# Kernel tuning notes

Hardware: AMD Instinct MI355X
Metric: run time of the kernel (lower is better)

## Reference

```python
import jax, jax.numpy as jnp
import numpy as np
from jax import lax

B, T_HIST, T_PRED = 8192, 11, 80
IN, H = 2, 64


def _glorot(key, shape, fan):
    bound = 1.0 / np.sqrt(fan)
    return jax.random.uniform(key, shape, jnp.float32, -bound, bound)


def setup_inputs() -> dict:
    key = jax.random.key(0)
    ks = jax.random.split(key, 20)
    inp = {"x": jax.random.normal(ks[0], (B, T_HIST, IN), jnp.float32)}
    # encoder / decoder: 2-layer tanh RNN, PyTorch param layout (out_features first)
    for pfx, base in (("enc", 1), ("dec", 9)):
        inp[f"{pfx}_Wih0"] = _glorot(ks[base + 0], (H, IN), H)
        inp[f"{pfx}_Whh0"] = _glorot(ks[base + 1], (H, H), H)
        inp[f"{pfx}_bih0"] = _glorot(ks[base + 2], (H,), H)
        inp[f"{pfx}_bhh0"] = _glorot(ks[base + 3], (H,), H)
        inp[f"{pfx}_Wih1"] = _glorot(ks[base + 4], (H, H), H)
        inp[f"{pfx}_Whh1"] = _glorot(ks[base + 5], (H, H), H)
        inp[f"{pfx}_bih1"] = _glorot(ks[base + 6], (H,), H)
        inp[f"{pfx}_bhh1"] = _glorot(ks[base + 7], (H,), H)
    inp["fc_W"] = _glorot(ks[17], (2, H), H)
    inp["fc_b"] = _glorot(ks[18], (2,), H)
    return inp


def _rnn_layer(x_seq, h0, Wih, Whh, bih, bhh):
    # x_seq: [T, B, in]; tanh RNN cell, returns (h_T, all hidden states [T, B, H])
    def step(h, x_t):
        h_new = jnp.tanh(x_t @ Wih.T + bih + h @ Whh.T + bhh)
        return h_new, h_new
    return lax.scan(step, h0, x_seq)


def reference(x,
              enc_Wih0, enc_Whh0, enc_bih0, enc_bhh0,
              enc_Wih1, enc_Whh1, enc_bih1, enc_bhh1,
              dec_Wih0, dec_Whh0, dec_bih0, dec_bhh0,
              dec_Wih1, dec_Whh1, dec_bih1, dec_bhh1,
              fc_W, fc_b):
    b = x.shape[0]
    h0 = jnp.zeros((b, H), x.dtype)
    x_seq = jnp.swapaxes(x, 0, 1)  # [T, B, 2]
    # encoder (dropout inactive in eval)
    h1_T, hs0 = _rnn_layer(x_seq, h0, enc_Wih0, enc_Whh0, enc_bih0, enc_bhh0)
    h2_T, _ = _rnn_layer(hs0, h0, enc_Wih1, enc_Whh1, enc_bih1, enc_bhh1)

    def dec_step(carry, _):
        h1, h2, inp = carry
        h1 = jnp.tanh(inp @ dec_Wih0.T + dec_bih0 + h1 @ dec_Whh0.T + dec_bhh0)
        h2 = jnp.tanh(h1 @ dec_Wih1.T + dec_bih1 + h2 @ dec_Whh1.T + dec_bhh1)
        pred = h2 @ fc_W.T + fc_b  # [B, 2]
        return (h1, h2, pred), pred

    init = (h1_T, h2_T, x[:, -1, :])
    _, preds = lax.scan(dec_step, init, None, length=T_PRED)  # [80, B, 2]
    return jnp.swapaxes(preds, 0, 1)  # [B, 80, 2]
```

## Files before the change

### kernel.cpp

```cpp
#include <hip/hip_runtime.h>

typedef __attribute__((ext_vector_type(8))) _Float16 f16x8;
typedef __attribute__((ext_vector_type(4))) float   f32x4;

namespace {
constexpr int kB    = 8192;
constexpr int kTH   = 11;
constexpr int kTP   = 80;
constexpr int kM    = 16;
constexpr int kStrH = 72;
}

__device__ __forceinline__ f16x8 cvt8(const float* f) {
    f16x8 v;
#pragma unroll
    for (int j = 0; j < 8; ++j) v[j] = (_Float16)f[j];
    return v;
}

__device__ __forceinline__ void loadB1(const float* __restrict__ W, int col, int q,
                                       f16x8 (&Bf)[2]) {
#pragma unroll
    for (int c = 0; c < 2; ++c) {
        const float* src = W + col * 64 + c * 32 + q * 8;
        const float4 a = reinterpret_cast<const float4*>(src)[0];
        const float4 b = reinterpret_cast<const float4*>(src)[1];
        float f[8] = {a.x, a.y, a.z, a.w, b.x, b.y, b.z, b.w};
        Bf[c] = cvt8(f);
    }
}

__device__ __forceinline__ void loadBfc(const float* __restrict__ fcW, int p, int q,
                                        f16x8 (&Bf)[2]) {
#pragma unroll
    for (int c = 0; c < 2; ++c) {
        float f[8];
#pragma unroll
        for (int j = 0; j < 8; ++j)
            f[j] = (p < 2) ? fcW[p * 64 + c * 32 + q * 8 + j] : 0.f;
        Bf[c] = cvt8(f);
    }
}

__device__ __forceinline__ void loadBG(const float* __restrict__ fcW, float w0, float w1,
                                       int q, f16x8 (&Bf)[2]) {
#pragma unroll
    for (int c = 0; c < 2; ++c) {
        float f[8];
#pragma unroll
        for (int j = 0; j < 8; ++j) {
            const int k = c * 32 + q * 8 + j;
            f[j] = w0 * fcW[k] + w1 * fcW[64 + k];
        }
        Bf[c] = cvt8(f);
    }
}

__device__ __forceinline__ f16x8 read_frag(const _Float16* plane, int off) {
    return *reinterpret_cast<const f16x8*>(plane + off);
}

__device__ __forceinline__ f32x4 mfma1(f16x8 a, f16x8 b, f32x4 acc) {
    return __builtin_amdgcn_mfma_f32_16x16x32_f16(a, b, acc, 0, 0, 0);
}

__device__ __forceinline__ float fast_tanh(float x) {
    const float e = __builtin_amdgcn_exp2f(x * 2.8853900817779268f);
    return fmaf(-2.0f, __builtin_amdgcn_rcpf(e + 1.0f), 1.0f);
}

__global__ __attribute__((amdgpu_waves_per_eu(2, 2))) __launch_bounds__(256)
void traj_rnn_kernel(
    const float* __restrict__ x,
    const float* __restrict__ eWih0, const float* __restrict__ eWhh0,
    const float* __restrict__ ebih0, const float* __restrict__ ebhh0,
    const float* __restrict__ eWih1, const float* __restrict__ eWhh1,
    const float* __restrict__ ebih1, const float* __restrict__ ebhh1,
    const float* __restrict__ dWih0, const float* __restrict__ dWhh0,
    const float* __restrict__ dbih0, const float* __restrict__ dbhh0,
    const float* __restrict__ dWih1, const float* __restrict__ dWhh1,
    const float* __restrict__ dbih1, const float* __restrict__ dbhh1,
    const float* __restrict__ fcW, const float* __restrict__ fcb,
    float* __restrict__ out)
{
    const int tid  = threadIdx.x;
    const int wv   = tid >> 6;
    const int lane = tid & 63;
    const int p    = lane & 15;
    const int q    = lane >> 4;
    const int col  = wv * 16 + p;
    const int r0   = blockIdx.x * kM;

    __shared__ __align__(16) _Float16 Hhi1[kM * kStrH];
    __shared__ __align__(16) _Float16 Hhi2[kM * kStrH];
    __shared__ __align__(16) float xbuf[kM * kTH * 2];
    __shared__ __align__(16) float predbuf[kM * kTP * 2];

    for (int i = tid; i < kM * kTH * 2; i += 256)
        xbuf[i] = x[r0 * (kTH * 2) + i];

    f16x8 H1f[2], H2f[2];
#pragma unroll
    for (int c = 0; c < 2; ++c) {
        H1f[c] = f16x8{0, 0, 0, 0, 0, 0, 0, 0};
        H2f[c] = f16x8{0, 0, 0, 0, 0, 0, 0, 0};
    }
    __syncthreads();

    if ((blockIdx.x ^ (blockIdx.x >> 3) ^ (blockIdx.x >> 8)) & 1) {
        __builtin_amdgcn_s_sleep(7);
        __builtin_amdgcn_s_sleep(7);
    }

    const int aoff = p * kStrH;

    {
        const float b0 = ebih0[col] + ebhh0[col];
        const float b1 = ebih1[col] + ebhh1[col];
        const float w0 = eWih0[col * 2 + 0];
        const float w1 = eWih0[col * 2 + 1];
        f16x8 B0[2], B1[2], B2[2];
        loadB1(eWhh0, col, q, B0);
        loadB1(eWih1, col, q, B1);
        loadB1(eWhh1, col, q, B2);

        f32x4 P1 = {b0, b0, b0, b0};

#pragma unroll 1
        for (int t = 0; t < kTH; ++t) {
            __builtin_amdgcn_s_setprio(1);
#pragma unroll
            for (int r = 0; r < 4; ++r) {
                const float2 xv = *reinterpret_cast<const float2*>(
                    &xbuf[(4 * q + r) * (kTH * 2) + 2 * t]);
                const float h1 = fast_tanh(fmaf(w0, xv.x, fmaf(w1, xv.y, P1[r])));
                Hhi1[(4 * q + r) * kStrH + col] = (_Float16)h1;
            }
            __builtin_amdgcn_s_setprio(0);
            f32x4 a2 = {b1, b1, b1, b1};
            a2 = mfma1(H2f[0], B2[0], a2);
            a2 = mfma1(H2f[1], B2[1], a2);
            __syncthreads();

            __builtin_amdgcn_s_setprio(1);
            H1f[0] = read_frag(Hhi1, aoff + q * 8);
            H1f[1] = read_frag(Hhi1, aoff + 32 + q * 8);
            a2 = mfma1(H1f[0], B1[0], a2);
            a2 = mfma1(H1f[1], B1[1], a2);
#pragma unroll
            for (int r = 0; r < 4; ++r) {
                const float h2 = fast_tanh(a2[r]);
                Hhi2[(4 * q + r) * kStrH + col] = (_Float16)h2;
            }
            __builtin_amdgcn_s_setprio(0);
            f32x4 np = {b0, b0, b0, b0};
            np = mfma1(H1f[0], B0[0], np);
            np = mfma1(H1f[1], B0[1], np);
            __syncthreads();

            __builtin_amdgcn_s_setprio(1);
            H2f[0] = read_frag(Hhi2, aoff + q * 8);
            H2f[1] = read_frag(Hhi2, aoff + 32 + q * 8);
            __builtin_amdgcn_s_setprio(0);
            P1 = np;
        }
    }

    {
        const float b0 = dbih0[col] + dbhh0[col];
        const float b1 = dbih1[col] + dbhh1[col];
        const float w0 = dWih0[col * 2 + 0];
        const float w1 = dWih0[col * 2 + 1];
        const float fb0 = fcb[0];
        const float fb1 = fcb[1];
        const float b0p = b0 + w0 * fb0 + w1 * fb1;
        const float fbp = (p == 0) ? fb0 : fb1;
        f16x8 B0[2], B1[2], B2[2], BF[2], BG[2];
        loadB1(dWhh0, col, q, B0);
        loadB1(dWih1, col, q, B1);
        loadB1(dWhh1, col, q, B2);
        loadBfc(fcW, p, q, BF);
        loadBG(fcW, w0, w1, q, BG);

        f32x4 P1 = {b0, b0, b0, b0};
        P1 = mfma1(H1f[0], B0[0], P1);
        P1 = mfma1(H1f[1], B0[1], P1);
#pragma unroll
        for (int r = 0; r < 4; ++r) {
            const float2 xv = *reinterpret_cast<const float2*>(
                &xbuf[(4 * q + r) * (kTH * 2) + 2 * (kTH - 1)]);
            P1[r] = fmaf(w0, xv.x, fmaf(w1, xv.y, P1[r]));
        }

#pragma unroll 2
        for (int t = 0; t < kTP; ++t) {
            __builtin_amdgcn_s_setprio(1);
#pragma unroll
            for (int r = 0; r < 4; ++r) {
                const float h1 = fast_tanh(P1[r]);
                Hhi1[(4 * q + r) * kStrH + col] = (_Float16)h1;
            }
            __builtin_amdgcn_s_setprio(0);
            f32x4 a2 = {b1, b1, b1, b1};
            a2 = mfma1(H2f[0], B2[0], a2);
            a2 = mfma1(H2f[1], B2[1], a2);
            __syncthreads();

            __builtin_amdgcn_s_setprio(1);
            H1f[0] = read_frag(Hhi1, aoff + q * 8);
            H1f[1] = read_frag(Hhi1, aoff + 32 + q * 8);
            a2 = mfma1(H1f[0], B1[0], a2);
            a2 = mfma1(H1f[1], B1[1], a2);
#pragma unroll
            for (int r = 0; r < 4; ++r) {
                const float h2 = fast_tanh(a2[r]);
                Hhi2[(4 * q + r) * kStrH + col] = (_Float16)h2;
            }
            __builtin_amdgcn_s_setprio(0);
            f32x4 nb = {0.f, 0.f, 0.f, 0.f};
            nb = mfma1(H1f[0], B0[0], nb);
            nb = mfma1(H1f[1], B0[1], nb);
            __syncthreads();

            __builtin_amdgcn_s_setprio(1);
            H2f[0] = read_frag(Hhi2, aoff + q * 8);
            H2f[1] = read_frag(Hhi2, aoff + 32 + q * 8);
            f32x4 ng = {b0p, b0p, b0p, b0p};
            ng = mfma1(H2f[0], BG[0], ng);
            ng = mfma1(H2f[1], BG[1], ng);
            P1 = ng + nb;
            __builtin_amdgcn_s_setprio(0);

            f32x4 fcC = {0.f, 0.f, 0.f, 0.f};
            fcC = mfma1(H2f[0], BF[0], fcC);
            fcC = mfma1(H2f[1], BF[1], fcC);
            if (wv == 0 && p < 2) {
#pragma unroll
                for (int r = 0; r < 4; ++r)
                    predbuf[((4 * q + r) * kTP + t) * 2 + p] = fcC[r] + fbp;
            }
        }
    }

    __syncthreads();
    {
        float4* dst = reinterpret_cast<float4*>(out + r0 * (kTP * 2));
        const float4* src = reinterpret_cast<const float4*>(predbuf);
        for (int i = tid; i < kM * kTP * 2 / 4; i += 256)
            dst[i] = src[i];
    }
}

extern "C" void kernel_launch(void* const* d_in, const int* in_sizes, int n_in,
                              void* d_out, int out_size, void* d_ws, size_t ws_size,
                              hipStream_t stream) {
    const float* x     = (const float*)d_in[0];
    const float* eWih0 = (const float*)d_in[1];
    const float* eWhh0 = (const float*)d_in[2];
    const float* ebih0 = (const float*)d_in[3];
    const float* ebhh0 = (const float*)d_in[4];
    const float* eWih1 = (const float*)d_in[5];
    const float* eWhh1 = (const float*)d_in[6];
    const float* ebih1 = (const float*)d_in[7];
    const float* ebhh1 = (const float*)d_in[8];
    const float* dWih0 = (const float*)d_in[9];
    const float* dWhh0 = (const float*)d_in[10];
    const float* dbih0 = (const float*)d_in[11];
    const float* dbhh0 = (const float*)d_in[12];
    const float* dWih1 = (const float*)d_in[13];
    const float* dWhh1 = (const float*)d_in[14];
    const float* dbih1 = (const float*)d_in[15];
    const float* dbhh1 = (const float*)d_in[16];
    const float* fcW   = (const float*)d_in[17];
    const float* fcb   = (const float*)d_in[18];
    float* out = (float*)d_out;

    dim3 grid(kB / kM);
    dim3 block(256);
    traj_rnn_kernel<<<grid, block, 0, stream>>>(
        x, eWih0, eWhh0, ebih0, ebhh0, eWih1, eWhh1, ebih1, ebhh1,
        dWih0, dWhh0, dbih0, dbhh0, dWih1, dWhh1, dbih1, dbhh1,
        fcW, fcb, out);
}
```

Measured before the change: 144.9 us.

## Replace block barriers with per-wave LDS flag spin-waits and double-buffered hidden states

```diff
diff --git a/kernel.cpp b/kernel.cpp
--- a/kernel.cpp
+++ b/kernel.cpp
@@ -67,6 +67,22 @@
 __device__ __forceinline__ float fast_tanh(float x) {
     const float e = __builtin_amdgcn_exp2f(x * 2.8853900817779268f);
     return fmaf(-2.0f, __builtin_amdgcn_rcpf(e + 1.0f), 1.0f);
+}
+
+__device__ __forceinline__ void publish(volatile int* f, int wv, int lane, int sv) {
+    asm volatile("s_waitcnt lgkmcnt(0)" ::: "memory");
+    if (lane == 0) f[wv] = sv;
+}
+
+__device__ __forceinline__ void spin_ge(const volatile int* f, int target) {
+    int guard = 0;
+    while (true) {
+        asm volatile("" ::: "memory");
+        const int m = min(min(f[0], f[1]), min(f[2], f[3]));
+        if (m >= target) break;
+        if (++guard > (1 << 22)) break;
+    }
+    asm volatile("" ::: "memory");
 }
 
 __global__ __attribute__((amdgpu_waves_per_eu(2, 2))) __launch_bounds__(256)
@@ -91,13 +107,16 @@
     const int col  = wv * 16 + p;
     const int r0   = blockIdx.x * kM;
 
-    __shared__ __align__(16) _Float16 Hhi1[kM * kStrH];
-    __shared__ __align__(16) _Float16 Hhi2[kM * kStrH];
+    __shared__ __align__(16) _Float16 H1s[2][kM * kStrH];
+    __shared__ __align__(16) _Float16 H2s[2][kM * kStrH];
     __shared__ __align__(16) float xbuf[kM * kTH * 2];
     __shared__ __align__(16) float predbuf[kM * kTP * 2];
+    __shared__ __align__(16) int p1f[4];
+    __shared__ __align__(16) int p2f[4];
 
     for (int i = tid; i < kM * kTH * 2; i += 256)
         xbuf[i] = x[r0 * (kTH * 2) + i];
+    if (tid < 4) { p1f[tid] = 0; p2f[tid] = 0; }
 
     f16x8 H1f[2], H2f[2];
 #pragma unroll
@@ -106,11 +125,6 @@
         H2f[c] = f16x8{0, 0, 0, 0, 0, 0, 0, 0};
     }
     __syncthreads();
-
-    if ((blockIdx.x ^ (blockIdx.x >> 3) ^ (blockIdx.x >> 8)) & 1) {
-        __builtin_amdgcn_s_sleep(7);
-        __builtin_amdgcn_s_sleep(7);
-    }
 
     const int aoff = p * kStrH;
 
@@ -128,40 +142,39 @@
 
 #pragma unroll 1
         for (int t = 0; t < kTH; ++t) {
-            __builtin_amdgcn_s_setprio(1);
+            const int sv = t + 1;
+            _Float16* h1p = H1s[sv & 1];
+            _Float16* h2p = H2s[sv & 1];
 #pragma unroll
             for (int r = 0; r < 4; ++r) {
                 const float2 xv = *reinterpret_cast<const float2*>(
                     &xbuf[(4 * q + r) * (kTH * 2) + 2 * t]);
                 const float h1 = fast_tanh(fmaf(w0, xv.x, fmaf(w1, xv.y, P1[r])));
-                Hhi1[(4 * q + r) * kStrH + col] = (_Float16)h1;
-            }
-            __builtin_amdgcn_s_setprio(0);
+                h1p[(4 * q + r) * kStrH + col] = (_Float16)h1;
+            }
+            publish(p1f, wv, lane, sv);
             f32x4 a2 = {b1, b1, b1, b1};
             a2 = mfma1(H2f[0], B2[0], a2);
             a2 = mfma1(H2f[1], B2[1], a2);
-            __syncthreads();
-
-            __builtin_amdgcn_s_setprio(1);
-            H1f[0] = read_frag(Hhi1, aoff + q * 8);
-            H1f[1] = read_frag(Hhi1, aoff + 32 + q * 8);
+            spin_ge(p1f, sv);
+
+            H1f[0] = read_frag(h1p, aoff + q * 8);
+            H1f[1] = read_frag(h1p, aoff + 32 + q * 8);
             a2 = mfma1(H1f[0], B1[0], a2);
             a2 = mfma1(H1f[1], B1[1], a2);
 #pragma unroll
             for (int r = 0; r < 4; ++r) {
                 const float h2 = fast_tanh(a2[r]);
-                Hhi2[(4 * q + r) * kStrH + col] = (_Float16)h2;
-            }
-            __builtin_amdgcn_s_setprio(0);
+                h2p[(4 * q + r) * kStrH + col] = (_Float16)h2;
+            }
+            publish(p2f, wv, lane, sv);
             f32x4 np = {b0, b0, b0, b0};
             np = mfma1(H1f[0], B0[0], np);
             np = mfma1(H1f[1], B0[1], np);
-            __syncthreads();
-
-            __builtin_amdgcn_s_setprio(1);
-            H2f[0] = read_frag(Hhi2, aoff + q * 8);
-            H2f[1] = read_frag(Hhi2, aoff + 32 + q * 8);
-            __builtin_amdgcn_s_setprio(0);
+            spin_ge(p2f, sv);
+
+            H2f[0] = read_frag(h2p, aoff + q * 8);
+            H2f[1] = read_frag(h2p, aoff + 32 + q * 8);
             P1 = np;
         }
     }
@@ -194,42 +207,41 @@
 
 #pragma unroll 2
         for (int t = 0; t < kTP; ++t) {
-            __builtin_amdgcn_s_setprio(1);
+            const int sv = kTH + 1 + t;
+            _Float16* h1p = H1s[sv & 1];
+            _Float16* h2p = H2s[sv & 1];
 #pragma unroll
             for (int r = 0; r < 4; ++r) {
                 const float h1 = fast_tanh(P1[r]);
-                Hhi1[(4 * q + r) * kStrH + col] = (_Float16)h1;
-            }
-            __builtin_amdgcn_s_setprio(0);
+                h1p[(4 * q + r) * kStrH + col] = (_Float16)h1;
+            }
+            publish(p1f, wv, lane, sv);
             f32x4 a2 = {b1, b1, b1, b1};
             a2 = mfma1(H2f[0], B2[0], a2);
             a2 = mfma1(H2f[1], B2[1], a2);
-            __syncthreads();
-
-            __builtin_amdgcn_s_setprio(1);
-            H1f[0] = read_frag(Hhi1, aoff + q * 8);
-            H1f[1] = read_frag(Hhi1, aoff + 32 + q * 8);
+            spin_ge(p1f, sv);
+
+            H1f[0] = read_frag(h1p, aoff + q * 8);
+            H1f[1] = read_frag(h1p, aoff + 32 + q * 8);
             a2 = mfma1(H1f[0], B1[0], a2);
             a2 = mfma1(H1f[1], B1[1], a2);
 #pragma unroll
             for (int r = 0; r < 4; ++r) {
                 const float h2 = fast_tanh(a2[r]);
-                Hhi2[(4 * q + r) * kStrH + col] = (_Float16)h2;
-            }
-            __builtin_amdgcn_s_setprio(0);
+                h2p[(4 * q + r) * kStrH + col] = (_Float16)h2;
+            }
+            publish(p2f, wv, lane, sv);
             f32x4 nb = {0.f, 0.f, 0.f, 0.f};
             nb = mfma1(H1f[0], B0[0], nb);
             nb = mfma1(H1f[1], B0[1], nb);
-            __syncthreads();
-
-            __builtin_amdgcn_s_setprio(1);
-            H2f[0] = read_frag(Hhi2, aoff + q * 8);
-            H2f[1] = read_frag(Hhi2, aoff + 32 + q * 8);
+            spin_ge(p2f, sv);
+
+            H2f[0] = read_frag(h2p, aoff + q * 8);
+            H2f[1] = read_frag(h2p, aoff + 32 + q * 8);
             f32x4 ng = {b0p, b0p, b0p, b0p};
             ng = mfma1(H2f[0], BG[0], ng);
             ng = mfma1(H2f[1], BG[1], ng);
             P1 = ng + nb;
-            __builtin_amdgcn_s_setprio(0);
 
             f32x4 fcC = {0.f, 0.f, 0.f, 0.f};
             fcC = mfma1(H2f[0], BF[0], fcC);
```

After: 180.0 us. +24.2%, slower.
